# Kernel optimization log

Measured on AMD Instinct MI355X. Metric: run time of the kernel, lower is better.

## Reference

```python
import jax, jax.numpy as jnp
import numpy as np

D = 128        # embed_d
L = 2          # n_layers
B = 4096       # batch of center nodes (drugs)
S = 10         # num_samples per neighbor type (hard-coded in node_het_agg)
NUM_CELLS, NUM_DRUGS, NUM_GENES = 2000, 4000, 20000
DRUG_F, GENE_F = 1024, 2048
NT = 3         # node types: cell, drug, gene


def setup_inputs() -> dict:
    key = jax.random.key(0)
    ks = jax.random.split(key, 16)
    s = 0.02
    inp = {
        # raw per-type feature tables (feature_loader / embedding table)
        "drug_feats": jax.random.normal(ks[0], (NUM_DRUGS, DRUG_F), jnp.float32),
        "gene_feats": jax.random.normal(ks[1], (NUM_GENES, GENE_F), jnp.float32),
        "cell_tab": jax.random.normal(ks[2], (NUM_CELLS, D), jnp.float32) * s,
        # feat_proj linears
        "W_drug": jax.random.normal(ks[3], (DRUG_F, D), jnp.float32) * s,
        "b_drug": jnp.zeros((D,), jnp.float32),
        "W_gene": jax.random.normal(ks[4], (GENE_F, D), jnp.float32) * s,
        "b_gene": jnp.zeros((D,), jnp.float32),
        # RnnGnnLayer params: per layer, per neighbor type, a simple tanh RNN
        "rnn_Wx": jax.random.normal(ks[5], (L, NT, D, D), jnp.float32) * s,
        "rnn_Wh": jax.random.normal(ks[6], (L, NT, D, D), jnp.float32) * s,
        "rnn_b": jnp.zeros((L, NT, D), jnp.float32),
        # per-layer attention vector over [self || candidate]
        "att_w": jax.random.normal(ks[7], (L, 2 * D), jnp.float32) * s,
        # center node ids (drug type) and pre-sampled neighbor ids per layer/type
        "center_ids": jax.random.randint(ks[8], (B,), 0, NUM_DRUGS, jnp.int32),
        "cell_neigh": jax.random.randint(ks[9], (L, B, S), 0, NUM_CELLS, jnp.int32),
        "drug_neigh": jax.random.randint(ks[10], (L, B, S), 0, NUM_DRUGS, jnp.int32),
        "gene_neigh": jax.random.randint(ks[11], (L, B, S), 0, NUM_GENES, jnp.int32),
    }
    return inp


def reference(drug_feats, gene_feats, cell_tab, W_drug, b_drug, W_gene, b_gene,
              rnn_Wx, rnn_Wh, rnn_b, att_w,
              center_ids, cell_neigh, drug_neigh, gene_neigh):
    # conteng_agg per node type: gather raw features then project to embed_d
    def emb_cell(idx):
        return cell_tab[idx]                              # [..., D]

    def emb_drug(idx):
        return drug_feats[idx] @ W_drug + b_drug          # gather [..., DRUG_F] -> [..., D]

    def emb_gene(idx):
        return gene_feats[idx] @ W_gene + b_gene

    def rnn_agg(x, Wx, Wh, b):
        # x: [B, S, D]; simple tanh RNN over the S sampled neighbors, last hidden
        def step(h, xt):
            h = jnp.tanh(xt @ Wx + h @ Wh + b)
            return h, None
        h0 = jnp.zeros((x.shape[0], Wx.shape[1]), x.dtype)
        h_last, _ = jax.lax.scan(step, h0, jnp.swapaxes(x, 0, 1))
        return h_last                                      # [B, D]

    h = emb_drug(center_ids)                               # initial center embeds [B, D]
    n_layers = rnn_Wx.shape[0]
    for l in range(n_layers):
        neigh = [(cell_neigh[l], emb_cell), (drug_neigh[l], emb_drug), (gene_neigh[l], emb_gene)]
        aggs = []
        for t, (idx, emb) in enumerate(neigh):
            x = emb(idx)                                   # [B, S, D]
            aggs.append(rnn_agg(x, rnn_Wx[l, t], rnn_Wh[l, t], rnn_b[l, t]))
        cands = jnp.stack([h] + aggs, axis=1)              # [B, 1+NT, D]
        self_b = jnp.broadcast_to(h[:, None, :], cands.shape)
        scores = jax.nn.leaky_relu(jnp.concatenate([self_b, cands], axis=-1) @ att_w[l])  # [B, 1+NT]
        alpha = jax.nn.softmax(scores, axis=1)
        h = jnp.einsum('bc,bcd->bd', alpha, cands)         # attention-weighted combine
    return h                                               # [B, D]
```

## Files before the change

### kernel.cpp

```cpp
#include <hip/hip_runtime.h>
#include <stdint.h>

#define D 128
#define Ssz 10
#define WP 136

typedef uint16_t u16;
typedef uint32_t u32;
typedef __attribute__((ext_vector_type(8))) short short8;
typedef __attribute__((ext_vector_type(4))) float f32x4;

#define AS1U32(p) ((const __attribute__((address_space(1))) u32*)(p))
#define AS3U32(p) ((__attribute__((address_space(3))) u32*)(p))

__device__ __forceinline__ u16 f2bf(float f){
  u32 x = __float_as_uint(f);
  return (u16)((x + 0x7fffu + ((x >> 16) & 1u)) >> 16);
}
__device__ __forceinline__ float bf2f(u16 u){ return __uint_as_float(((u32)u) << 16); }

__global__ __launch_bounds__(256) void transpose_k(const float* __restrict__ W,
                                                   u16* __restrict__ WT, int K){
  int i = blockIdx.x * 256 + threadIdx.x;
  if (i >= K * D) return;
  int n = i / K, k = i - n * K;
  WT[i] = f2bf(W[k * D + n]);
}

__global__ __launch_bounds__(256) void cvt_bf16(const float* __restrict__ in,
                                                u16* __restrict__ out, int n2){
  int i = blockIdx.x * 256 + threadIdx.x;
  if (i >= n2) return;
  float v0 = in[2 * i], v1 = in[2 * i + 1];
  ((u32*)out)[i] = (u32)f2bf(v0) | ((u32)f2bf(v1) << 16);
}

__global__ __launch_bounds__(256) void proj_gemm(
    const float* __restrict__ feats, int K, int M,
    const u16* __restrict__ WT,
    const float* __restrict__ bias,
    u16* __restrict__ outb,
    float* __restrict__ outf)
{
  __shared__ u16 Bt[128 * 128];

  int lane = threadIdx.x & 63;
  int wave = threadIdx.x >> 6;
  int quad = lane >> 4, l16 = lane & 15;
  int m0 = blockIdx.x * 64 + wave * 16;

  int row = min(m0 + l16, M - 1);
  const float* aptr = feats + (long)row * K + quad * 8;

  int st_nrow = wave * 32 + (lane >> 4);
  int st_p    = lane & 15;

  f32x4 acc[8];
#pragma unroll
  for (int nt = 0; nt < 8; ++nt){
    float bv = bias[nt * 16 + l16];
    f32x4 t = {bv, bv, bv, bv};
    acc[nt] = t;
  }

  f32x4 afA[4][2], afB[4][2];
#pragma unroll
  for (int ks = 0; ks < 4; ++ks){
    afA[ks][0] = *(const f32x4*)(aptr + ks * 32);
    afA[ks][1] = *(const f32x4*)(aptr + ks * 32 + 4);
  }

  auto chunk_step = [&](f32x4 (&acur)[4][2], f32x4 (&anxt)[4][2], int kc) {
#pragma unroll
    for (int j = 0; j < 8; ++j){
      int n = st_nrow + j * 4;
      int c = st_p ^ (n & 15);
      const u16* g = WT + (long)n * K + kc + c * 8;
      __builtin_amdgcn_global_load_lds(AS1U32(g),
                                       AS3U32(&Bt[(wave * 8 + j) * 512]),
                                       16, 0, 0);
    }
    if (kc + 128 < K){
#pragma unroll
      for (int ks = 0; ks < 4; ++ks){
        anxt[ks][0] = *(const f32x4*)(aptr + kc + 128 + ks * 32);
        anxt[ks][1] = *(const f32x4*)(aptr + kc + 128 + ks * 32 + 4);
      }
    }
    __syncthreads();

#pragma unroll
    for (int ks = 0; ks < 4; ++ks){
      short8 a;
#pragma unroll
      for (int q = 0; q < 4; ++q){
        a[q]     = (short)f2bf(acur[ks][0][q]);
        a[4 + q] = (short)f2bf(acur[ks][1][q]);
      }
#pragma unroll
      for (int nt = 0; nt < 8; ++nt){
        int n = nt * 16 + l16;
        int p = (ks * 4 + quad) ^ l16;
        short8 b = *(const short8*)(&Bt[n * 128 + p * 8]);
        acc[nt] = __builtin_amdgcn_mfma_f32_16x16x32_bf16(a, b, acc[nt], 0, 0, 0);
      }
    }
    __syncthreads();
  };

  for (int kc = 0; kc < K; kc += 256){
    chunk_step(afA, afB, kc);
    chunk_step(afB, afA, kc + 128);
  }

#pragma unroll
  for (int nt = 0; nt < 8; ++nt){
    int col = nt * 16 + l16;
#pragma unroll
    for (int r = 0; r < 4; ++r){
      int mr = m0 + quad * 4 + r;
      if (mr < M){
        long o = (long)mr * D + col;
        if (outb) outb[o] = f2bf(acc[nt][r]);
        if (outf) outf[o] = acc[nt][r];
      }
    }
  }
}

__global__ __launch_bounds__(256) void gather_f32(
    const float* __restrict__ tab, const int* __restrict__ idx,
    float* __restrict__ out, int nrows, int ntab)
{
  int gt = blockIdx.x * 256 + threadIdx.x;
  int r = gt >> 6, c = gt & 63;
  if (r >= nrows) return;
  int row = min(max(idx[r], 0), ntab - 1);
  ((float2*)out)[(long)r * 64 + c] = ((const float2*)tab)[(long)row * 64 + c];
}

__global__ __launch_bounds__(256, 3) void rnn3_kernel(
    const u16* __restrict__ tab0, const u16* __restrict__ tab1,
    const u16* __restrict__ tab2,
    const int* __restrict__ idx0, const int* __restrict__ idx1,
    const int* __restrict__ idx2,
    const float* __restrict__ Wx,
    const float* __restrict__ Wh,
    const float* __restrict__ bvec,
    u16* __restrict__ agg, int CB)
{
  __shared__ u16 WT[D * WP];
  __shared__ u16 hbuf[16 * WP];

  int t = blockIdx.y;
  const u16* tab = (t == 0) ? tab0 : (t == 1) ? tab1 : tab2;
  const int* idx = (t == 0) ? idx0 : (t == 1) ? idx1 : idx2;
  const float* Wxp = Wx + (size_t)t * D * D;
  const float* Whp = Wh + (size_t)t * D * D;

  int tid = threadIdx.x;
  int lane = tid & 63, wave = tid >> 6;
  int quad = lane >> 4, l16 = lane & 15;
  int n0 = wave * 32;

  for (int i = tid; i < D * D; i += 256){
    int n = i >> 7, k = i & 127;
    WT[n * WP + k] = f2bf(Wxp[k * D + n]);
  }
  for (int i = tid; i < 16 * WP; i += 256) hbuf[i] = 0;
  __syncthreads();

  short8 wxf[2][4], whf[2][4];
#pragma unroll
  for (int nt = 0; nt < 2; ++nt){
    int n = n0 + nt * 16 + l16;
#pragma unroll
    for (int ks = 0; ks < 4; ++ks)
      wxf[nt][ks] = *(const short8*)(&WT[n * WP + ks * 32 + quad * 8]);
  }
  __syncthreads();
  for (int i = tid; i < D * D; i += 256){
    int n = i >> 7, k = i & 127;
    WT[n * WP + k] = f2bf(Whp[k * D + n]);
  }
  __syncthreads();
#pragma unroll
  for (int nt = 0; nt < 2; ++nt){
    int n = n0 + nt * 16 + l16;
#pragma unroll
    for (int ks = 0; ks < 4; ++ks)
      whf[nt][ks] = *(const short8*)(&WT[n * WP + ks * 32 + quad * 8]);
  }

  float bias0 = bvec[t * D + n0 + l16];
  float bias1 = bvec[t * D + n0 + 16 + l16];

  int b0 = blockIdx.x * 16;
  int nid[Ssz];
#pragma unroll
  for (int s = 0; s < Ssz; ++s) nid[s] = idx[(b0 + l16) * Ssz + s];

  short8 xc[4], xn[4];
  {
    const u16* xb = tab + (long)nid[0] * D + quad * 8;
#pragma unroll
    for (int ks = 0; ks < 4; ++ks) xc[ks] = *(const short8*)(xb + ks * 32);
  }

  for (int s = 0; s < Ssz; ++s){
    short8 hf[4];
#pragma unroll
    for (int ks = 0; ks < 4; ++ks)
      hf[ks] = *(const short8*)(&hbuf[l16 * WP + ks * 32 + quad * 8]);
    if (s + 1 < Ssz){
      const u16* xb = tab + (long)nid[s + 1] * D + quad * 8;
#pragma unroll
      for (int ks = 0; ks < 4; ++ks) xn[ks] = *(const short8*)(xb + ks * 32);
    }
    f32x4 acc0 = {bias0, bias0, bias0, bias0};
    f32x4 acc1 = {bias1, bias1, bias1, bias1};
#pragma unroll
    for (int ks = 0; ks < 4; ++ks){
      acc0 = __builtin_amdgcn_mfma_f32_16x16x32_bf16(xc[ks], wxf[0][ks], acc0, 0, 0, 0);
      acc0 = __builtin_amdgcn_mfma_f32_16x16x32_bf16(hf[ks], whf[0][ks], acc0, 0, 0, 0);
      acc1 = __builtin_amdgcn_mfma_f32_16x16x32_bf16(xc[ks], wxf[1][ks], acc1, 0, 0, 0);
      acc1 = __builtin_amdgcn_mfma_f32_16x16x32_bf16(hf[ks], whf[1][ks], acc1, 0, 0, 0);
    }
    __syncthreads();
#pragma unroll
    for (int r = 0; r < 4; ++r){
      float v0 = tanhf(acc0[r]);
      float v1 = tanhf(acc1[r]);
      hbuf[(quad * 4 + r) * WP + n0 + l16]      = f2bf(v0);
      hbuf[(quad * 4 + r) * WP + n0 + 16 + l16] = f2bf(v1);
      if (s == Ssz - 1){
        long row = (long)t * CB + b0 + quad * 4 + r;
        agg[row * D + n0 + l16]      = f2bf(v0);
        agg[row * D + n0 + 16 + l16] = f2bf(v1);
      }
    }
    __syncthreads();
#pragma unroll
    for (int ks = 0; ks < 4; ++ks) xc[ks] = xn[ks];
  }
}

__global__ __launch_bounds__(256) void att_kernel(
    const float* __restrict__ h,
    const u16* __restrict__ agg,
    const float* __restrict__ aw,
    float* __restrict__ out,
    int CB)
{
  int gt = blockIdx.x * 256 + threadIdx.x;
  int lane = gt & 63;
  int b = gt >> 6;
  int e = 2 * lane;

  float c[4][2];
  c[0][0] = h[(long)b * D + e];
  c[0][1] = h[(long)b * D + e + 1];
#pragma unroll
  for (int t = 0; t < 3; ++t){
    c[t + 1][0] = bf2f(agg[((long)t * CB + b) * D + e]);
    c[t + 1][1] = bf2f(agg[((long)t * CB + b) * D + e + 1]);
  }
  float as0 = aw[e],     as1 = aw[e + 1];
  float ac0 = aw[D + e], ac1 = aw[D + e + 1];

  float selfp = c[0][0] * as0 + c[0][1] * as1;
  float sc[4];
#pragma unroll
  for (int cc = 0; cc < 4; ++cc) sc[cc] = selfp + c[cc][0] * ac0 + c[cc][1] * ac1;
#pragma unroll
  for (int off = 32; off >= 1; off >>= 1){
#pragma unroll
    for (int cc = 0; cc < 4; ++cc) sc[cc] += __shfl_xor(sc[cc], off, 64);
  }
#pragma unroll
  for (int cc = 0; cc < 4; ++cc) sc[cc] = sc[cc] > 0.f ? sc[cc] : 0.01f * sc[cc];

  float mx = fmaxf(fmaxf(sc[0], sc[1]), fmaxf(sc[2], sc[3]));
  float ex[4], ssum = 0.f;
#pragma unroll
  for (int cc = 0; cc < 4; ++cc){ ex[cc] = expf(sc[cc] - mx); ssum += ex[cc]; }
  float o0 = 0.f, o1 = 0.f;
#pragma unroll
  for (int cc = 0; cc < 4; ++cc){
    float a = ex[cc] / ssum;
    o0 += a * c[cc][0];
    o1 += a * c[cc][1];
  }
  out[(long)b * D + e]     = o0;
  out[(long)b * D + e + 1] = o1;
}

extern "C" void kernel_launch(void* const* d_in, const int* in_sizes, int n_in,
                              void* d_out, int out_size, void* d_ws, size_t ws_size,
                              hipStream_t stream)
{
  const float* drug_feats = (const float*)d_in[0];
  const float* gene_feats = (const float*)d_in[1];
  const float* cell_tab   = (const float*)d_in[2];
  const float* W_drug     = (const float*)d_in[3];
  const float* b_drug     = (const float*)d_in[4];
  const float* W_gene     = (const float*)d_in[5];
  const float* b_gene     = (const float*)d_in[6];
  const float* rnn_Wx     = (const float*)d_in[7];
  const float* rnn_Wh     = (const float*)d_in[8];
  const float* rnn_b      = (const float*)d_in[9];
  const float* att_w      = (const float*)d_in[10];
  const int* center_ids   = (const int*)d_in[11];
  const int* cell_neigh   = (const int*)d_in[12];
  const int* drug_neigh   = (const int*)d_in[13];
  const int* gene_neigh   = (const int*)d_in[14];

  u16* ws     = (u16*)d_ws;
  u16* WdT    = ws;
  u16* WgT    = WdT + 131072;
  u16* cellT  = WgT + 262144;
  u16* drugPb = cellT + 256000;
  u16* genePb = drugPb + 512000;
  float* drugPf = (float*)(genePb + 2560000);
  u16* agg    = (u16*)(drugPf + 512000);

  int CB = 4096;
  while (CB > 64){
    size_t need = 9490432u + (size_t)768 * CB;
    if (need <= ws_size) break;
    CB >>= 1;
  }
  float* h = (float*)d_out;

  transpose_k<<<(1024 * D + 255) / 256, 256, 0, stream>>>(W_drug, WdT, 1024);
  transpose_k<<<(2048 * D + 255) / 256, 256, 0, stream>>>(W_gene, WgT, 2048);
  cvt_bf16<<<(2000 * 64 + 255) / 256, 256, 0, stream>>>(cell_tab, cellT, 2000 * 64);

  proj_gemm<<<(4000 + 63) / 64, 256, 0, stream>>>(drug_feats, 1024, 4000,
                                                  WdT, b_drug, drugPb, drugPf);
  proj_gemm<<<(20000 + 63) / 64, 256, 0, stream>>>(gene_feats, 2048, 20000,
                                                   WgT, b_gene, genePb,
                                                   (float*)nullptr);

  for (int b0 = 0; b0 < 4096; b0 += CB){
    gather_f32<<<CB / 4, 256, 0, stream>>>(drugPf, center_ids + b0,
                                           h + (size_t)b0 * D, CB, 4000);
    for (int l = 0; l < 2; ++l){
      const int* cn = cell_neigh + ((size_t)l * 4096 + b0) * Ssz;
      const int* dn = drug_neigh + ((size_t)l * 4096 + b0) * Ssz;
      const int* gn = gene_neigh + ((size_t)l * 4096 + b0) * Ssz;

      rnn3_kernel<<<dim3(CB / 16, 3), 256, 0, stream>>>(
          cellT, drugPb, genePb, cn, dn, gn,
          rnn_Wx + (size_t)l * 3 * D * D,
          rnn_Wh + (size_t)l * 3 * D * D,
          rnn_b  + (size_t)l * 3 * D,
          agg, CB);

      att_kernel<<<CB / 4, 256, 0, stream>>>(h + (size_t)b0 * D, agg,
                                             att_w + (size_t)l * 2 * D,
                                             h + (size_t)b0 * D, CB);
    }
  }
}
```

Baseline: 440.8 us.

## Precompute input projections per table row and batch both layers' RNNs

The x@Wx+b term is now computed once per embedding-table row for both layers (26000 rows x 2) by a new MFMA GEMM, so the RNN kernel only does h@Wh and gathers the precomputed fp32 rows. Both layers' RNNs run in a single launch, since neighbor embeddings do not depend on h. Weight transposes move to a one-time pre-pass instead of being redone per block. tanhf becomes an exp-based approximation. This costs a larger workspace and a dense GEMM over all table rows, including rows that are never sampled.

```diff
diff --git a/kernel.cpp b/kernel.cpp
--- a/kernel.cpp
+++ b/kernel.cpp
@@ -3,7 +3,7 @@
 
 #define D 128
 #define Ssz 10
-#define WP 136
+#define HP 136
 
 typedef uint16_t u16;
 typedef uint32_t u32;
@@ -18,6 +18,11 @@
   return (u16)((x + 0x7fffu + ((x >> 16) & 1u)) >> 16);
 }
 __device__ __forceinline__ float bf2f(u16 u){ return __uint_as_float(((u32)u) << 16); }
+
+__device__ __forceinline__ float ftanh(float x){
+  float e = __expf(2.0f * x);
+  return 1.0f - 2.0f / (e + 1.0f);
+}
 
 __global__ __launch_bounds__(256) void transpose_k(const float* __restrict__ W,
                                                    u16* __restrict__ WT, int K){
@@ -25,6 +30,13 @@
   if (i >= K * D) return;
   int n = i / K, k = i - n * K;
   WT[i] = f2bf(W[k * D + n]);
+}
+
+__global__ __launch_bounds__(256) void transpose_b6(const float* __restrict__ W,
+                                                    u16* __restrict__ WT){
+  int i = blockIdx.x * 256 + threadIdx.x;
+  int j = i & 16383, n = j >> 7, k = j & 127;
+  WT[i] = f2bf(W[(i & ~16383) + k * D + n]);
 }
 
 __global__ __launch_bounds__(256) void cvt_bf16(const float* __restrict__ in,
@@ -128,6 +140,59 @@
   }
 }
 
+__global__ __launch_bounds__(256) void xw_gemm(
+    const u16* __restrict__ cellT, const u16* __restrict__ drugPb,
+    const u16* __restrict__ genePb,
+    const u16* __restrict__ WxT6,
+    const float* __restrict__ bvec,
+    float* __restrict__ xwb)
+{
+  int bx = blockIdx.x, l = blockIdx.y;
+  int t, m0, M, rbase;
+  const u16* tab;
+  if (bx < 32)      { t = 0; m0 = bx * 64;        M = 2000;  rbase = 0;    tab = cellT; }
+  else if (bx < 95) { t = 1; m0 = (bx - 32) * 64; M = 4000;  rbase = 2000; tab = drugPb; }
+  else              { t = 2; m0 = (bx - 95) * 64; M = 20000; rbase = 6000; tab = genePb; }
+  int mat = l * 3 + t;
+  const u16* WT = WxT6 + (size_t)mat * 16384;
+
+  int lane = threadIdx.x & 63, wave = threadIdx.x >> 6;
+  int quad = lane >> 4, l16 = lane & 15;
+  int mt = m0 + wave * 16;
+  int mr = min(mt + l16, M - 1);
+
+  short8 a[4];
+#pragma unroll
+  for (int ks = 0; ks < 4; ++ks)
+    a[ks] = *(const short8*)(tab + (long)mr * D + ks * 32 + quad * 8);
+
+  f32x4 acc[8];
+#pragma unroll
+  for (int nt = 0; nt < 8; ++nt){
+    float bv = bvec[mat * D + nt * 16 + l16];
+    f32x4 tv = {bv, bv, bv, bv};
+    acc[nt] = tv;
+  }
+#pragma unroll
+  for (int nt = 0; nt < 8; ++nt){
+#pragma unroll
+    for (int ks = 0; ks < 4; ++ks){
+      short8 b = *(const short8*)(WT + (nt * 16 + l16) * D + ks * 32 + quad * 8);
+      acc[nt] = __builtin_amdgcn_mfma_f32_16x16x32_bf16(a[ks], b, acc[nt], 0, 0, 0);
+    }
+  }
+#pragma unroll
+  for (int nt = 0; nt < 8; ++nt){
+    int col = nt * 16 + l16;
+#pragma unroll
+    for (int r = 0; r < 4; ++r){
+      int mrow = mt + quad * 4 + r;
+      if (mrow < M)
+        xwb[((long)l * 26000 + rbase + mrow) * D + col] = acc[nt][r];
+    }
+  }
+}
+
 __global__ __launch_bounds__(256) void gather_f32(
     const float* __restrict__ tab, const int* __restrict__ idx,
     float* __restrict__ out, int nrows, int ntab)
@@ -139,110 +204,106 @@
   ((float2*)out)[(long)r * 64 + c] = ((const float2*)tab)[(long)row * 64 + c];
 }
 
-__global__ __launch_bounds__(256, 3) void rnn3_kernel(
-    const u16* __restrict__ tab0, const u16* __restrict__ tab1,
-    const u16* __restrict__ tab2,
-    const int* __restrict__ idx0, const int* __restrict__ idx1,
-    const int* __restrict__ idx2,
-    const float* __restrict__ Wx,
-    const float* __restrict__ Wh,
-    const float* __restrict__ bvec,
+__global__ __launch_bounds__(256, 3) void rnn6_kernel(
+    const float* __restrict__ xwb,
+    const u16* __restrict__ WhT6,
+    const int* __restrict__ cn, const int* __restrict__ dn,
+    const int* __restrict__ gn,
+    int b0,
     u16* __restrict__ agg, int CB)
 {
-  __shared__ u16 WT[D * WP];
-  __shared__ u16 hbuf[16 * WP];
-
-  int t = blockIdx.y;
-  const u16* tab = (t == 0) ? tab0 : (t == 1) ? tab1 : tab2;
-  const int* idx = (t == 0) ? idx0 : (t == 1) ? idx1 : idx2;
-  const float* Wxp = Wx + (size_t)t * D * D;
-  const float* Whp = Wh + (size_t)t * D * D;
-
-  int tid = threadIdx.x;
-  int lane = tid & 63, wave = tid >> 6;
+  __shared__ u16 hbuf[16 * HP];
+
+  int t = blockIdx.y, l = blockIdx.z;
+  const int* idx = (t == 0) ? cn : (t == 1) ? dn : gn;
+  int rbase = (t == 0) ? 0 : (t == 1) ? 2000 : 6000;
+  int nmax  = (t == 0) ? 2000 : (t == 1) ? 4000 : 20000;
+  const float* xw = xwb + ((size_t)l * 26000 + rbase) * D;
+  const u16* WT = WhT6 + (size_t)(l * 3 + t) * 16384;
+
+  int tid = threadIdx.x, lane = tid & 63, wave = tid >> 6;
   int quad = lane >> 4, l16 = lane & 15;
   int n0 = wave * 32;
 
-  for (int i = tid; i < D * D; i += 256){
-    int n = i >> 7, k = i & 127;
-    WT[n * WP + k] = f2bf(Wxp[k * D + n]);
-  }
-  for (int i = tid; i < 16 * WP; i += 256) hbuf[i] = 0;
-  __syncthreads();
-
-  short8 wxf[2][4], whf[2][4];
+  short8 whf[2][4];
 #pragma unroll
   for (int nt = 0; nt < 2; ++nt){
     int n = n0 + nt * 16 + l16;
 #pragma unroll
     for (int ks = 0; ks < 4; ++ks)
-      wxf[nt][ks] = *(const short8*)(&WT[n * WP + ks * 32 + quad * 8]);
-  }
+      whf[nt][ks] = *(const short8*)(WT + n * D + ks * 32 + quad * 8);
+  }
+
+  for (int i = tid; i < 16 * HP; i += 256) hbuf[i] = 0;
+
+  int brow = blockIdx.x * 16;
+  const int* ip = idx + ((size_t)l * 4096 + b0 + brow + quad * 4) * Ssz;
+  long arow = ((long)(l * 3 + t) * CB + brow) * D;
+
+  int nidA[4], nidB[4];
+  float xwA[8], xwB[8];
+#pragma unroll
+  for (int r = 0; r < 4; ++r) nidA[r] = min(max(ip[r * Ssz], 0), nmax - 1);
+#pragma unroll
+  for (int r = 0; r < 4; ++r){
+    const float* p = xw + (long)nidA[r] * D + n0 + l16;
+    xwA[r] = p[0]; xwA[4 + r] = p[16];
+  }
+#pragma unroll
+  for (int r = 0; r < 4; ++r) nidB[r] = min(max(ip[r * Ssz + 1], 0), nmax - 1);
   __syncthreads();
-  for (int i = tid; i < D * D; i += 256){
-    int n = i >> 7, k = i & 127;
-    WT[n * WP + k] = f2bf(Whp[k * D + n]);
-  }
-  __syncthreads();
-#pragma unroll
-  for (int nt = 0; nt < 2; ++nt){
-    int n = n0 + nt * 16 + l16;
+
+  auto step = [&](int s, float (&xwc)[8], int (&nidn)[4],
+                  float (&xwn)[8], int (&nidf)[4]){
+    if (s + 1 < Ssz){
+#pragma unroll
+      for (int r = 0; r < 4; ++r){
+        const float* p = xw + (long)nidn[r] * D + n0 + l16;
+        xwn[r] = p[0]; xwn[4 + r] = p[16];
+      }
+    }
+    if (s + 2 < Ssz){
+#pragma unroll
+      for (int r = 0; r < 4; ++r)
+        nidf[r] = min(max(ip[r * Ssz + s + 2], 0), nmax - 1);
+    }
+    short8 hf[4];
 #pragma unroll
     for (int ks = 0; ks < 4; ++ks)
-      whf[nt][ks] = *(const short8*)(&WT[n * WP + ks * 32 + quad * 8]);
-  }
-
-  float bias0 = bvec[t * D + n0 + l16];
-  float bias1 = bvec[t * D + n0 + 16 + l16];
-
-  int b0 = blockIdx.x * 16;
-  int nid[Ssz];
-#pragma unroll
-  for (int s = 0; s < Ssz; ++s) nid[s] = idx[(b0 + l16) * Ssz + s];
-
-  short8 xc[4], xn[4];
-  {
-    const u16* xb = tab + (long)nid[0] * D + quad * 8;
-#pragma unroll
-    for (int ks = 0; ks < 4; ++ks) xc[ks] = *(const short8*)(xb + ks * 32);
-  }
-
-  for (int s = 0; s < Ssz; ++s){
-    short8 hf[4];
-#pragma unroll
-    for (int ks = 0; ks < 4; ++ks)
-      hf[ks] = *(const short8*)(&hbuf[l16 * WP + ks * 32 + quad * 8]);
-    if (s + 1 < Ssz){
-      const u16* xb = tab + (long)nid[s + 1] * D + quad * 8;
-#pragma unroll
-      for (int ks = 0; ks < 4; ++ks) xn[ks] = *(const short8*)(xb + ks * 32);
-    }
-    f32x4 acc0 = {bias0, bias0, bias0, bias0};
-    f32x4 acc1 = {bias1, bias1, bias1, bias1};
+      hf[ks] = *(const short8*)(&hbuf[l16 * HP + ks * 32 + quad * 8]);
+    f32x4 acc0 = {xwc[0], xwc[1], xwc[2], xwc[3]};
+    f32x4 acc1 = {xwc[4], xwc[5], xwc[6], xwc[7]};
 #pragma unroll
     for (int ks = 0; ks < 4; ++ks){
-      acc0 = __builtin_amdgcn_mfma_f32_16x16x32_bf16(xc[ks], wxf[0][ks], acc0, 0, 0, 0);
       acc0 = __builtin_amdgcn_mfma_f32_16x16x32_bf16(hf[ks], whf[0][ks], acc0, 0, 0, 0);
-      acc1 = __builtin_amdgcn_mfma_f32_16x16x32_bf16(xc[ks], wxf[1][ks], acc1, 0, 0, 0);
       acc1 = __builtin_amdgcn_mfma_f32_16x16x32_bf16(hf[ks], whf[1][ks], acc1, 0, 0, 0);
     }
     __syncthreads();
 #pragma unroll
     for (int r = 0; r < 4; ++r){
-      float v0 = tanhf(acc0[r]);
-      float v1 = tanhf(acc1[r]);
-      hbuf[(quad * 4 + r) * WP + n0 + l16]      = f2bf(v0);
-      hbuf[(quad * 4 + r) * WP + n0 + 16 + l16] = f2bf(v1);
+      float v0 = ftanh(acc0[r]);
+      float v1 = ftanh(acc1[r]);
+      hbuf[(quad * 4 + r) * HP + n0 + l16]      = f2bf(v0);
+      hbuf[(quad * 4 + r) * HP + n0 + 16 + l16] = f2bf(v1);
       if (s == Ssz - 1){
-        long row = (long)t * CB + b0 + quad * 4 + r;
-        agg[row * D + n0 + l16]      = f2bf(v0);
-        agg[row * D + n0 + 16 + l16] = f2bf(v1);
+        long o = arow + (long)(quad * 4 + r) * D;
+        agg[o + n0 + l16]      = f2bf(v0);
+        agg[o + n0 + 16 + l16] = f2bf(v1);
       }
     }
     __syncthreads();
-#pragma unroll
-    for (int ks = 0; ks < 4; ++ks) xc[ks] = xn[ks];
-  }
+  };
+
+  step(0, xwA, nidB, xwB, nidA);
+  step(1, xwB, nidA, xwA, nidB);
+  step(2, xwA, nidB, xwB, nidA);
+  step(3, xwB, nidA, xwA, nidB);
+  step(4, xwA, nidB, xwB, nidA);
+  step(5, xwB, nidA, xwA, nidB);
+  step(6, xwA, nidB, xwB, nidA);
+  step(7, xwB, nidA, xwA, nidB);
+  step(8, xwA, nidB, xwB, nidA);
+  step(9, xwB, nidA, xwA, nidB);
 }
 
 __global__ __launch_bounds__(256) void att_kernel(
@@ -318,46 +379,46 @@
   u16* ws     = (u16*)d_ws;
   u16* WdT    = ws;
   u16* WgT    = WdT + 131072;
-  u16* cellT  = WgT + 262144;
+  u16* WxT6   = WgT + 262144;
+  u16* WhT6   = WxT6 + 98304;
+  u16* cellT  = WhT6 + 98304;
   u16* drugPb = cellT + 256000;
   u16* genePb = drugPb + 512000;
   float* drugPf = (float*)(genePb + 2560000);
-  u16* agg    = (u16*)(drugPf + 512000);
+  float* xwb    = drugPf + 512000;
+  u16* agg      = (u16*)(xwb + 6656000);
 
   int CB = 4096;
   while (CB > 64){
-    size_t need = 9490432u + (size_t)768 * CB;
+    size_t need = 36507648u + (size_t)1536 * CB;
     if (need <= ws_size) break;
     CB >>= 1;
   }
   float* h = (float*)d_out;
 
-  transpose_k<<<(1024 * D + 255) / 256, 256, 0, stream>>>(W_drug, WdT, 1024);
-  transpose_k<<<(2048 * D + 255) / 256, 256, 0, stream>>>(W_gene, WgT, 2048);
-  cvt_bf16<<<(2000 * 64 + 255) / 256, 256, 0, stream>>>(cell_tab, cellT, 2000 * 64);
-
-  proj_gemm<<<(4000 + 63) / 64, 256, 0, stream>>>(drug_feats, 1024, 4000,
-                                                  WdT, b_drug, drugPb, drugPf);
-  proj_gemm<<<(20000 + 63) / 64, 256, 0, stream>>>(gene_feats, 2048, 20000,
-                                                   WgT, b_gene, genePb,
-                                                   (float*)nullptr);
+  transpose_k<<<512, 256, 0, stream>>>(W_drug, WdT, 1024);
+  transpose_k<<<1024, 256, 0, stream>>>(W_gene, WgT, 2048);
+  transpose_b6<<<384, 256, 0, stream>>>(rnn_Wx, WxT6);
+  transpose_b6<<<384, 256, 0, stream>>>(rnn_Wh, WhT6);
+  cvt_bf16<<<500, 256, 0, stream>>>(cell_tab, cellT, 2000 * 64);
+
+  proj_gemm<<<63, 256, 0, stream>>>(drug_feats, 1024, 4000,
+                                    WdT, b_drug, drugPb, drugPf);
+  proj_gemm<<<313, 256, 0, stream>>>(gene_feats, 2048, 20000,
+                                     WgT, b_gene, genePb, (float*)nullptr);
+
+  xw_gemm<<<dim3(408, 2), 256, 0, stream>>>(cellT, drugPb, genePb,
+                                            WxT6, rnn_b, xwb);
 
   for (int b0 = 0; b0 < 4096; b0 += CB){
     gather_f32<<<CB / 4, 256, 0, stream>>>(drugPf, center_ids + b0,
                                            h + (size_t)b0 * D, CB, 4000);
+    rnn6_kernel<<<dim3(CB / 16, 3, 2), 256, 0, stream>>>(
+        xwb, WhT6, cell_neigh, drug_neigh, gene_neigh, b0, agg, CB);
+
     for (int l = 0; l < 2; ++l){
-      const int* cn = cell_neigh + ((size_t)l * 4096 + b0) * Ssz;
-      const int* dn = drug_neigh + ((size_t)l * 4096 + b0) * Ssz;
-      const int* gn = gene_neigh + ((size_t)l * 4096 + b0) * Ssz;
-
-      rnn3_kernel<<<dim3(CB / 16, 3), 256, 0, stream>>>(
-          cellT, drugPb, genePb, cn, dn, gn,
-          rnn_Wx + (size_t)l * 3 * D * D,
-          rnn_Wh + (size_t)l * 3 * D * D,
-          rnn_b  + (size_t)l * 3 * D,
-          agg, CB);
-
-      att_kernel<<<CB / 4, 256, 0, stream>>>(h + (size_t)b0 * D, agg,
+      att_kernel<<<CB / 4, 256, 0, stream>>>(h + (size_t)b0 * D,
+                                             agg + (size_t)l * 3 * CB * D,
                                              att_w + (size_t)l * 2 * D,
                                              h + (size_t)b0 * D, CB);
     }
```

New measurement: 366.7 us. 16.8% less time.
